# Kernel optimization log

Hardware: AMD Instinct MI355X
Metric: run time of the kernel (lower is better)

## Reference

```python
import jax, jax.numpy as jnp
import numpy as np

B, S, D_IN, D_OUT, R = 4, 1024, 1024, 1024, 8

def setup_inputs() -> dict:
    key = jax.random.key(0)
    k1, k2, k3, k4, k5 = jax.random.split(key, 5)
    scale = 1.0 / np.sqrt(D_IN)
    return {
        "x": jax.random.normal(k1, (B, S, D_IN), dtype=jnp.float32),
        "A_params": jax.random.normal(k2, (B, S, D_OUT, R), dtype=jnp.float32) * 0.02,
        "B_params": jax.random.normal(k3, (B, S, R, D_IN), dtype=jnp.float32) * 0.02,
        "W": jax.random.normal(k4, (D_OUT, D_IN), dtype=jnp.float32) * scale,
        "b": jax.random.normal(k5, (D_OUT,), dtype=jnp.float32) * scale,
    }

def reference(x, A_params, B_params, W, b):
    # base linear: y = x @ W^T + b  -> [B, S, D_OUT]
    base_out = jnp.einsum('bsi,oi->bso', x, W) + b
    # per-token low-rank update: (x @ B^T) @ A^T
    inter = jnp.einsum('bsi,bsri->bsr', x, B_params)           # [B, S, R]
    adaptation = jnp.einsum('bsr,bsor->bso', inter, A_params)  # [B, S, D_OUT]
    return base_out + adaptation
```

## Files before the change

kernel.cpp:

```cpp
#include <hip/hip_runtime.h>
#include <hip/hip_bf16.h>
#include <stdint.h>

#define TOKENS 4096
#define DIN 1024
#define DOUT 1024
#define RANK 8

typedef __attribute__((ext_vector_type(4))) float f32x4;
typedef __attribute__((ext_vector_type(8))) short short8;

__device__ __forceinline__ unsigned short f2bf(float f) {
    union { float f; unsigned u; } v; v.f = f;
    unsigned r = v.u + 0x7FFFu + ((v.u >> 16) & 1u);
    return (unsigned short)(r >> 16);
}

__global__ __launch_bounds__(256) void k_convert_w(const float* __restrict__ W,
                                                   ushort* __restrict__ Wb) {
    int i = blockIdx.x * 256 + threadIdx.x;
    float4 v = ((const float4*)W)[i];
    ushort4 u;
    u.x = f2bf(v.x); u.y = f2bf(v.y); u.z = f2bf(v.z); u.w = f2bf(v.w);
    ((ushort4*)Wb)[i] = u;
}

__global__ __launch_bounds__(256) void k_inter(const float* __restrict__ x,
                                               const float* __restrict__ Bp,
                                               float* __restrict__ inter,
                                               ushort* __restrict__ xb) {
    const int t = blockIdx.x;
    const int tid = threadIdx.x;
    const int lane = tid & 63, wave = tid >> 6;

    float4 xv = ((const float4*)(x + (size_t)t * DIN))[tid];

    ushort4 u;
    u.x = f2bf(xv.x); u.y = f2bf(xv.y); u.z = f2bf(xv.z); u.w = f2bf(xv.w);
    ((ushort4*)(xb + (size_t)t * DIN))[tid] = u;

    const float4* B4 = (const float4*)(Bp + (size_t)t * RANK * DIN);
    float acc[RANK];
#pragma unroll
    for (int r = 0; r < RANK; ++r) {
        float4 bv = B4[r * 256 + tid];
        acc[r] = xv.x * bv.x + xv.y * bv.y + xv.z * bv.z + xv.w * bv.w;
    }

    __shared__ float part[4][RANK];
#pragma unroll
    for (int r = 0; r < RANK; ++r) {
        float v = acc[r];
#pragma unroll
        for (int off = 32; off > 0; off >>= 1) v += __shfl_xor(v, off, 64);
        if (lane == 0) part[wave][r] = v;
    }
    __syncthreads();
    if (tid < RANK)
        inter[(size_t)t * RANK + tid] =
            part[0][tid] + part[1][tid] + part[2][tid] + part[3][tid];
}

__global__ __launch_bounds__(256) void k_gemm_fused(const ushort* __restrict__ Xb,
                                                    const ushort* __restrict__ Wb,
                                                    const float* __restrict__ bias,
                                                    const float* __restrict__ inter,
                                                    const float* __restrict__ Ap,
                                                    float* __restrict__ out) {
    __shared__ ushort As[128 * 64];
    __shared__ ushort Bs[64 * 64];
    __shared__ float sInter[128 * 8];
    __shared__ float sBias[64];
    __shared__ float sums[32 * 256];

    const int tid = threadIdx.x;
    const int lane = tid & 63, wave = tid >> 6;
    const int wm = wave >> 1, wn = wave & 1;
    const int M0 = blockIdx.y * 128;
    const int N0 = blockIdx.x * 64;
    const int col16 = lane & 15;
    const int kg = lane >> 4;

    ((float4*)sInter)[tid] = ((const float4*)(inter + (size_t)M0 * RANK))[tid];
    if (tid < 16) ((float4*)sBias)[tid] = ((const float4*)(bias + N0))[tid];

    const float* Abase = Ap + ((size_t)(M0 + wm * 64 + kg * 4) * DOUT +
                               (N0 + wn * 32 + col16)) * RANK;

    f32x4 acc[4][2] = {};

    for (int it = 0; it < 16; ++it) {
        const int kt = it * 64;
        __syncthreads();
#pragma unroll
        for (int st = 0; st < 4; ++st) {
            int flat = st * 256 + tid;
            int row = flat >> 3, ch = flat & 7;
            const ushort* g = Xb + (size_t)(M0 + row) * DIN + kt + ch * 8;
            __builtin_amdgcn_global_load_lds(
                (const __attribute__((address_space(1))) void*)g,
                (__attribute__((address_space(3))) void*)(As + flat * 8), 16, 0, 0);
        }
#pragma unroll
        for (int st = 0; st < 2; ++st) {
            int flat = st * 256 + tid;
            int row = flat >> 3, ch = flat & 7;
            const ushort* g = Wb + (size_t)(N0 + row) * DIN + kt + ch * 8;
            __builtin_amdgcn_global_load_lds(
                (const __attribute__((address_space(1))) void*)g,
                (__attribute__((address_space(3))) void*)(Bs + flat * 8), 16, 0, 0);
        }

        const int nf = it >> 3, mf = (it >> 1) & 3, rg0 = (it & 1) * 2;
        const float* Ae0 = Abase + ((size_t)(mf * 16 + rg0) * DOUT + nf * 16) * RANK;
        const float* Ae1 = Ae0 + (size_t)DOUT * RANK;
        float4 a00 = ((const float4*)Ae0)[0];
        float4 a01 = ((const float4*)Ae0)[1];
        float4 a10 = ((const float4*)Ae1)[0];
        float4 a11 = ((const float4*)Ae1)[1];

        asm volatile("s_waitcnt vmcnt(0)" ::: "memory");
        __syncthreads();

#pragma unroll
        for (int ks = 0; ks < 2; ++ks) {
            short8 a[4], b[2];
#pragma unroll
            for (int m4 = 0; m4 < 4; ++m4)
                a[m4] = *(const short8*)(As + (wm * 64 + m4 * 16 + col16) * 64 + ks * 32 + kg * 8);
#pragma unroll
            for (int n2 = 0; n2 < 2; ++n2)
                b[n2] = *(const short8*)(Bs + (wn * 32 + n2 * 16 + col16) * 64 + ks * 32 + kg * 8);
#pragma unroll
            for (int m4 = 0; m4 < 4; ++m4)
#pragma unroll
                for (int n2 = 0; n2 < 2; ++n2)
                    acc[m4][n2] = __builtin_amdgcn_mfma_f32_16x16x32_bf16(
                        a[m4], b[n2], acc[m4][n2], 0, 0, 0);
        }

        const int mloc0 = wm * 64 + mf * 16 + kg * 4 + rg0;
        const float4* iv0 = (const float4*)(sInter + mloc0 * 8);
        const float4* iv1 = (const float4*)(sInter + (mloc0 + 1) * 8);
        float4 i00 = iv0[0], i01 = iv0[1], i10 = iv1[0], i11 = iv1[1];
        float d0 = a00.x * i00.x + a00.y * i00.y + a00.z * i00.z + a00.w * i00.w +
                   a01.x * i01.x + a01.y * i01.y + a01.z * i01.z + a01.w * i01.w;
        float d1 = a10.x * i10.x + a10.y * i10.y + a10.z * i10.z + a10.w * i10.w +
                   a11.x * i11.x + a11.y * i11.y + a11.z * i11.z + a11.w * i11.w;
        sums[(it * 2) * 256 + tid] = d0;
        sums[(it * 2 + 1) * 256 + tid] = d1;
    }

#pragma unroll
    for (int nf = 0; nf < 2; ++nf) {
        const int oc = wn * 32 + nf * 16 + col16;
        const int o = N0 + oc;
        const float bb = sBias[oc];
#pragma unroll
        for (int mf = 0; mf < 4; ++mf) {
#pragma unroll
            for (int rg = 0; rg < 4; ++rg) {
                const int m = M0 + wm * 64 + mf * 16 + kg * 4 + rg;
                const int e = nf * 16 + mf * 4 + rg;
                out[(size_t)m * DOUT + o] = acc[mf][nf][rg] + bb + sums[e * 256 + tid];
            }
        }
    }
}

extern "C" void kernel_launch(void* const* d_in, const int* in_sizes, int n_in,
                              void* d_out, int out_size, void* d_ws, size_t ws_size,
                              hipStream_t stream) {
    const float* x    = (const float*)d_in[0];
    const float* Ap   = (const float*)d_in[1];
    const float* Bp   = (const float*)d_in[2];
    const float* W    = (const float*)d_in[3];
    const float* bias = (const float*)d_in[4];
    float* out = (float*)d_out;

    ushort* xb = (ushort*)d_ws;
    ushort* Wb = xb + (size_t)TOKENS * DIN;
    float* inter = (float*)(Wb + (size_t)DOUT * DIN);

    hipLaunchKernelGGL(k_convert_w, dim3(DOUT * DIN / 1024), dim3(256), 0, stream, W, Wb);
    hipLaunchKernelGGL(k_inter, dim3(TOKENS), dim3(256), 0, stream, x, Bp, inter, xb);
    hipLaunchKernelGGL(k_gemm_fused, dim3(DOUT / 64, TOKENS / 128), dim3(256), 0, stream,
                       xb, Wb, bias, inter, Ap, out);
}
```

Baseline: 73.41 us.

## Double-buffer GEMM LDS tiles, fold adaptation into accumulators, swizzle block order

The fused GEMM kernel now keeps two LDS buffers for the X and W tiles and issues the next tile's global-to-LDS loads before computing on the current one, so load latency overlaps MFMA work. The low-rank adaptation dot products are added straight into the MFMA accumulator registers, which removes the 32 KB shared 'sums' array and frees LDS. The grid is flattened to 1D with a block-index swizzle so that consecutive blocks land on different M/N tiles, aiming at better L2 reuse. Adding into the accumulator mid-loop relies on the MFMA output register layout matching the adaptation element mapping, and the wait-then-barrier at the end of each iteration still serialises every step.

```diff
diff --git a/kernel.cpp b/kernel.cpp
--- a/kernel.cpp
+++ b/kernel.cpp
@@ -6,6 +6,9 @@
 #define DIN 1024
 #define DOUT 1024
 #define RANK 8
+#define BM 128
+#define BN 64
+#define BK 64
 
 typedef __attribute__((ext_vector_type(4))) float f32x4;
 typedef __attribute__((ext_vector_type(8))) short short8;
@@ -67,17 +70,20 @@
                                                     const float* __restrict__ inter,
                                                     const float* __restrict__ Ap,
                                                     float* __restrict__ out) {
-    __shared__ ushort As[128 * 64];
-    __shared__ ushort Bs[64 * 64];
-    __shared__ float sInter[128 * 8];
-    __shared__ float sBias[64];
-    __shared__ float sums[32 * 256];
+    __shared__ ushort As[2][BM * BK];
+    __shared__ ushort Bs[2][BN * BK];
+    __shared__ float sInter[BM * 8];
+    __shared__ float sBias[BN];
 
     const int tid = threadIdx.x;
     const int lane = tid & 63, wave = tid >> 6;
     const int wm = wave >> 1, wn = wave & 1;
-    const int M0 = blockIdx.y * 128;
-    const int N0 = blockIdx.x * 64;
+
+    const int bid = blockIdx.x;
+    const int swz = (bid & 7) * 64 + (bid >> 3);
+    const int M0 = (swz >> 4) * BM;
+    const int N0 = (swz & 15) * BN;
+
     const int col16 = lane & 15;
     const int kg = lane >> 4;
 
@@ -87,11 +93,7 @@
     const float* Abase = Ap + ((size_t)(M0 + wm * 64 + kg * 4) * DOUT +
                                (N0 + wn * 32 + col16)) * RANK;
 
-    f32x4 acc[4][2] = {};
-
-    for (int it = 0; it < 16; ++it) {
-        const int kt = it * 64;
-        __syncthreads();
+    auto stage = [&](int b, int kt) {
 #pragma unroll
         for (int st = 0; st < 4; ++st) {
             int flat = st * 256 + tid;
@@ -99,7 +101,7 @@
             const ushort* g = Xb + (size_t)(M0 + row) * DIN + kt + ch * 8;
             __builtin_amdgcn_global_load_lds(
                 (const __attribute__((address_space(1))) void*)g,
-                (__attribute__((address_space(3))) void*)(As + flat * 8), 16, 0, 0);
+                (__attribute__((address_space(3))) void*)(&As[b][flat * 8]), 16, 0, 0);
         }
 #pragma unroll
         for (int st = 0; st < 2; ++st) {
@@ -108,8 +110,20 @@
             const ushort* g = Wb + (size_t)(N0 + row) * DIN + kt + ch * 8;
             __builtin_amdgcn_global_load_lds(
                 (const __attribute__((address_space(1))) void*)g,
-                (__attribute__((address_space(3))) void*)(Bs + flat * 8), 16, 0, 0);
-        }
+                (__attribute__((address_space(3))) void*)(&Bs[b][flat * 8]), 16, 0, 0);
+        }
+    };
+
+    stage(0, 0);
+    asm volatile("s_waitcnt vmcnt(0) lgkmcnt(0)" ::: "memory");
+    __builtin_amdgcn_s_barrier();
+
+    f32x4 acc[4][2] = {};
+
+#pragma unroll
+    for (int it = 0; it < 16; ++it) {
+        const int cur = it & 1;
+        if (it < 15) stage(cur ^ 1, (it + 1) * BK);
 
         const int nf = it >> 3, mf = (it >> 1) & 3, rg0 = (it & 1) * 2;
         const float* Ae0 = Abase + ((size_t)(mf * 16 + rg0) * DOUT + nf * 16) * RANK;
@@ -119,18 +133,15 @@
         float4 a10 = ((const float4*)Ae1)[0];
         float4 a11 = ((const float4*)Ae1)[1];
 
-        asm volatile("s_waitcnt vmcnt(0)" ::: "memory");
-        __syncthreads();
-
 #pragma unroll
         for (int ks = 0; ks < 2; ++ks) {
             short8 a[4], b[2];
 #pragma unroll
             for (int m4 = 0; m4 < 4; ++m4)
-                a[m4] = *(const short8*)(As + (wm * 64 + m4 * 16 + col16) * 64 + ks * 32 + kg * 8);
+                a[m4] = *(const short8*)(&As[cur][(wm * 64 + m4 * 16 + col16) * BK + ks * 32 + kg * 8]);
 #pragma unroll
             for (int n2 = 0; n2 < 2; ++n2)
-                b[n2] = *(const short8*)(Bs + (wn * 32 + n2 * 16 + col16) * 64 + ks * 32 + kg * 8);
+                b[n2] = *(const short8*)(&Bs[cur][(wn * 32 + n2 * 16 + col16) * BK + ks * 32 + kg * 8]);
 #pragma unroll
             for (int m4 = 0; m4 < 4; ++m4)
 #pragma unroll
@@ -147,8 +158,11 @@
                    a01.x * i01.x + a01.y * i01.y + a01.z * i01.z + a01.w * i01.w;
         float d1 = a10.x * i10.x + a10.y * i10.y + a10.z * i10.z + a10.w * i10.w +
                    a11.x * i11.x + a11.y * i11.y + a11.z * i11.z + a11.w * i11.w;
-        sums[(it * 2) * 256 + tid] = d0;
-        sums[(it * 2 + 1) * 256 + tid] = d1;
+        acc[mf][nf][rg0] += d0;
+        acc[mf][nf][rg0 + 1] += d1;
+
+        asm volatile("s_waitcnt vmcnt(0)" ::: "memory");
+        __builtin_amdgcn_s_barrier();
     }
 
 #pragma unroll
@@ -161,8 +175,7 @@
 #pragma unroll
             for (int rg = 0; rg < 4; ++rg) {
                 const int m = M0 + wm * 64 + mf * 16 + kg * 4 + rg;
-                const int e = nf * 16 + mf * 4 + rg;
-                out[(size_t)m * DOUT + o] = acc[mf][nf][rg] + bb + sums[e * 256 + tid];
+                out[(size_t)m * DOUT + o] = acc[mf][nf][rg] + bb;
             }
         }
     }
@@ -184,6 +197,6 @@
 
     hipLaunchKernelGGL(k_convert_w, dim3(DOUT * DIN / 1024), dim3(256), 0, stream, W, Wb);
     hipLaunchKernelGGL(k_inter, dim3(TOKENS), dim3(256), 0, stream, x, Bp, inter, xb);
-    hipLaunchKernelGGL(k_gemm_fused, dim3(DOUT / 64, TOKENS / 128), dim3(256), 0, stream,
+    hipLaunchKernelGGL(k_gemm_fused, dim3((TOKENS / BM) * (DOUT / BN)), dim3(256), 0, stream,
                        xb, Wb, bias, inter, Ap, out);
 }
```

Result: no change. 73.29 us (-0.2%).
